# Kernel optimization log

Measured on AMD Instinct MI355X. Metric: run time of the kernel, lower is better.

The kernel has to match this reference:

```python
import jax, jax.numpy as jnp
import numpy as np

# BD-format field offsets (last dim = 512)
MARK_AX = 0
OPCODE_BASE = 16
OP_SHL = OPCODE_BASE + 23   # 39
OP_SHR = OPCODE_BASE + 24   # 40
ALU_LO = 64                 # 16-wide one-hot low nibble of operand
ALU_HI = 80                 # 16-wide one-hot high nibble of operand
AX_CARRY_LO = 96            # 16-wide one-hot shift amount
OUTPUT_LO = 128             # 16-wide result-low scatter target
OUTPUT_HI = 144             # 16-wide result-high scatter target

B, SEQ, D = 8, 32768, 512


def setup_inputs() -> dict:
    key = jax.random.key(0)
    ks = jax.random.split(key, 6)
    # background noise strictly below the 0.5 threshold so only intended bits fire
    x = jax.random.uniform(ks[0], (B, SEQ, D), dtype=jnp.float32) * 0.4
    mark = (jax.random.uniform(ks[1], (B, SEQ)) < 0.75).astype(jnp.float32)
    op_sel = jax.random.randint(ks[2], (B, SEQ), 0, 3)  # 0=none, 1=SHL, 2=SHR
    lo = jax.random.randint(ks[3], (B, SEQ), 0, 16)
    hi = jax.random.randint(ks[4], (B, SEQ), 0, 16)
    sa = jax.random.randint(ks[5], (B, SEQ), 0, 16)
    oh = lambda idx: jax.nn.one_hot(idx, 16, dtype=jnp.float32)
    x = x.at[..., MARK_AX].set(mark)
    x = x.at[..., OP_SHL].set((op_sel == 1).astype(jnp.float32))
    x = x.at[..., OP_SHR].set((op_sel == 2).astype(jnp.float32))
    x = x.at[..., ALU_LO:ALU_LO + 16].set(oh(lo))
    x = x.at[..., ALU_HI:ALU_HI + 16].set(oh(hi))
    x = x.at[..., AX_CARRY_LO:AX_CARRY_LO + 16].set(oh(sa))
    return {"x_bd": x}


def reference(x_bd):
    hot = x_bd > 0.5
    # 'first k with value > 0.5' == argmax over boolean (0 if none, matching torch default)
    first16 = lambda off: jnp.argmax(hot[..., off:off + 16], axis=-1).astype(jnp.int32)
    lo = first16(ALU_LO)          # [B,S] in [0,16)
    hi = first16(ALU_HI)
    sa = first16(AX_CARRY_LO)     # shift amount
    val = lo + 16 * hi            # 8-bit operand
    shl = jnp.left_shift(val, sa) & 0xFF   # SHL layer stack: 8-bit left shift
    shr = jnp.right_shift(val, sa)         # SHR layer stack: logical right shift
    mark = hot[..., MARK_AX]
    is_shl = hot[..., OP_SHL]
    is_shr = jnp.logical_and(hot[..., OP_SHR], jnp.logical_not(is_shl))  # elif priority
    act_shl = jnp.logical_and(mark, is_shl)
    act_shr = jnp.logical_and(mark, is_shr)
    active = jnp.logical_or(act_shl, act_shr)
    res = jnp.where(act_shl, shl, jnp.where(act_shr, shr, 0))
    res = jnp.clip(res, 0, 255)   # ge_to_bd clamps each nibble to [0,15]
    rlo = res & 15
    rhi = res >> 4
    amp = 2.0 * active.astype(x_bd.dtype)  # +2.0 scatter only for routed tokens
    add_lo = amp[..., None] * jax.nn.one_hot(rlo, 16, dtype=x_bd.dtype)
    add_hi = amp[..., None] * jax.nn.one_hot(rhi, 16, dtype=x_bd.dtype)
    out = x_bd.at[..., OUTPUT_LO:OUTPUT_LO + 16].add(add_lo)
    out = out.at[..., OUTPUT_HI:OUTPUT_HI + 16].add(add_hi)
    return out
```

## Files before the change

kernel.cpp:

```cpp
#include <hip/hip_runtime.h>

#define MARK_AX      0
#define OP_SHL       39
#define OP_SHR       40
#define ALU_LO       64
#define ALU_HI       80
#define AX_CARRY_LO  96
#define OUTPUT_LO    128
#define OUTPUT_HI    144

constexpr int D = 512;

__global__ __launch_bounds__(256) void shift_ffn_kernel(
    const float* __restrict__ x, float* __restrict__ out, int ntok)
{
    const int lane = threadIdx.x & 63;
    const int wid  = (blockIdx.x * blockDim.x + threadIdx.x) >> 6;
    const int nw   = (gridDim.x * blockDim.x) >> 6;
    const int e0   = 4 * lane;

    for (int tok = wid; tok < ntok; tok += nw) {
        const float* xt = x   + (size_t)tok * D;
        float*       ot = out + (size_t)tok * D;

        float4 a = *reinterpret_cast<const float4*>(xt + e0);
        float4 b = *reinterpret_cast<const float4*>(xt + 256 + e0);

        unsigned long long m = 0ull;
        if (lane < 28) {
            const float av[4] = {a.x, a.y, a.z, a.w};
            #pragma unroll
            for (int j = 0; j < 4; ++j) {
                const int e = e0 + j;
                if (av[j] > 0.5f) {
                    if (e == MARK_AX)                              m |= 1ull << 48;
                    else if (e == OP_SHL)                          m |= 1ull << 49;
                    else if (e == OP_SHR)                          m |= 1ull << 50;
                    else if (e >= ALU_LO      && e < ALU_LO + 16)  m |= 1ull << (e - ALU_LO);
                    else if (e >= ALU_HI      && e < ALU_HI + 16)  m |= 1ull << (e - ALU_HI + 16);
                    else if (e >= AX_CARRY_LO && e < AX_CARRY_LO+16) m |= 1ull << (e - AX_CARRY_LO + 32);
                }
            }
        }

        #pragma unroll
        for (int s = 1; s < 64; s <<= 1)
            m |= __shfl_xor(m, s, 64);

        const unsigned lo16 = (unsigned)( m        & 0xFFFFu);
        const unsigned hi16 = (unsigned)((m >> 16) & 0xFFFFu);
        const unsigned sa16 = (unsigned)((m >> 32) & 0xFFFFu);
        const int lo = lo16 ? (__ffs(lo16) - 1) : 0;
        const int hi = hi16 ? (__ffs(hi16) - 1) : 0;
        const int sa = sa16 ? (__ffs(sa16) - 1) : 0;

        const int  val     = lo + 16 * hi;
        const bool mark    = (m >> 48) & 1ull;
        const bool is_shl  = (m >> 49) & 1ull;
        const bool is_shr  = (((m >> 50) & 1ull) != 0) && !is_shl;
        const bool act_shl = mark && is_shl;
        const bool act_shr = mark && is_shr;
        const bool active  = act_shl || act_shr;

        int res = 0;
        if (act_shl)      res = (val << sa) & 0xFF;
        else if (act_shr) res = val >> sa;

        const int tlo = OUTPUT_LO + (res & 15);
        const int thi = OUTPUT_HI + (res >> 4);

        if (active) {
            float* ap = &a.x;
            #pragma unroll
            for (int j = 0; j < 4; ++j) {
                const int e = e0 + j;
                float add = 0.0f;
                if (e == tlo) add += 2.0f;
                if (e == thi) add += 2.0f;
                ap[j] += add;
            }
        }

        *reinterpret_cast<float4*>(ot + e0)       = a;
        *reinterpret_cast<float4*>(ot + 256 + e0) = b;
    }
}

extern "C" void kernel_launch(void* const* d_in, const int* in_sizes, int n_in,
                              void* d_out, int out_size, void* d_ws, size_t ws_size,
                              hipStream_t stream)
{
    const float* x = (const float*)d_in[0];
    float* out = (float*)d_out;
    const int ntok = in_sizes[0] / D;

    const int block = 256;
    const int grid  = 2048;
    shift_ffn_kernel<<<grid, block, 0, stream>>>(x, out, ntok);
}
```

Before: 209.9 us.

## Decode with wave ballots, process token pairs, use nontemporal loads/stores

```diff
diff --git a/kernel.cpp b/kernel.cpp
--- a/kernel.cpp
+++ b/kernel.cpp
@@ -11,6 +11,41 @@
 
 constexpr int D = 512;
 
+typedef float f32x4 __attribute__((ext_vector_type(4)));
+
+__device__ __forceinline__ int first_hot(const unsigned long long b[4], int lane0) {
+    int best = 999;
+    #pragma unroll
+    for (int j = 0; j < 4; ++j) {
+        unsigned nib = (unsigned)(b[j] >> lane0) & 0xFu;
+        int cand = nib ? (4 * (__ffs(nib) - 1) + j) : 999;
+        best = min(best, cand);
+    }
+    return (best >= 16) ? 0 : best;
+}
+
+__device__ __forceinline__ void decode(const unsigned long long b[4],
+                                       int& tlo, int& thi, float& amp) {
+    const bool mark = (b[0] >> 0) & 1ull;
+    const bool shl  = (b[3] >> 9) & 1ull;
+    const bool shr  = (b[0] >> 10) & 1ull;
+
+    const int lo = first_hot(b, 16);
+    const int hi = first_hot(b, 20);
+    const int sa = first_hot(b, 24);
+
+    const int  val     = lo + 16 * hi;
+    const bool act_shl = mark && shl;
+    const bool act_shr = mark && shr && !shl;
+
+    const int res = act_shl ? ((val << sa) & 0xFF)
+                  : (act_shr ? (val >> sa) : 0);
+
+    tlo = OUTPUT_LO + (res & 15);
+    thi = OUTPUT_HI + (res >> 4);
+    amp = (act_shl || act_shr) ? 2.0f : 0.0f;
+}
+
 __global__ __launch_bounds__(256) void shift_ffn_kernel(
     const float* __restrict__ x, float* __restrict__ out, int ntok)
 {
@@ -18,71 +53,38 @@
     const int wid  = (blockIdx.x * blockDim.x + threadIdx.x) >> 6;
     const int nw   = (gridDim.x * blockDim.x) >> 6;
     const int e0   = 4 * lane;
+    const int npair = ntok >> 1;
 
-    for (int tok = wid; tok < ntok; tok += nw) {
-        const float* xt = x   + (size_t)tok * D;
-        float*       ot = out + (size_t)tok * D;
+    for (int p = wid; p < npair; p += nw) {
+        const float* xt0 = x   + (size_t)(2 * p) * D;
+        float*       ot0 = out + (size_t)(2 * p) * D;
 
-        float4 a = *reinterpret_cast<const float4*>(xt + e0);
-        float4 b = *reinterpret_cast<const float4*>(xt + 256 + e0);
+        f32x4 a0 = __builtin_nontemporal_load((const f32x4*)(xt0 + e0));
+        f32x4 c0 = __builtin_nontemporal_load((const f32x4*)(xt0 + 256 + e0));
+        f32x4 a1 = __builtin_nontemporal_load((const f32x4*)(xt0 + D + e0));
+        f32x4 c1 = __builtin_nontemporal_load((const f32x4*)(xt0 + D + 256 + e0));
 
-        unsigned long long m = 0ull;
-        if (lane < 28) {
-            const float av[4] = {a.x, a.y, a.z, a.w};
-            #pragma unroll
-            for (int j = 0; j < 4; ++j) {
-                const int e = e0 + j;
-                if (av[j] > 0.5f) {
-                    if (e == MARK_AX)                              m |= 1ull << 48;
-                    else if (e == OP_SHL)                          m |= 1ull << 49;
-                    else if (e == OP_SHR)                          m |= 1ull << 50;
-                    else if (e >= ALU_LO      && e < ALU_LO + 16)  m |= 1ull << (e - ALU_LO);
-                    else if (e >= ALU_HI      && e < ALU_HI + 16)  m |= 1ull << (e - ALU_HI + 16);
-                    else if (e >= AX_CARRY_LO && e < AX_CARRY_LO+16) m |= 1ull << (e - AX_CARRY_LO + 32);
-                }
-            }
+        unsigned long long b0[4], b1[4];
+        #pragma unroll
+        for (int j = 0; j < 4; ++j) b0[j] = __ballot(a0[j] > 0.5f);
+        #pragma unroll
+        for (int j = 0; j < 4; ++j) b1[j] = __ballot(a1[j] > 0.5f);
+
+        int tlo0, thi0, tlo1, thi1; float amp0, amp1;
+        decode(b0, tlo0, thi0, amp0);
+        decode(b1, tlo1, thi1, amp1);
+
+        #pragma unroll
+        for (int j = 0; j < 4; ++j) {
+            const int e = e0 + j;
+            a0[j] += ((e == tlo0) ? amp0 : 0.0f) + ((e == thi0) ? amp0 : 0.0f);
+            a1[j] += ((e == tlo1) ? amp1 : 0.0f) + ((e == thi1) ? amp1 : 0.0f);
         }
 
-        #pragma unroll
-        for (int s = 1; s < 64; s <<= 1)
-            m |= __shfl_xor(m, s, 64);
-
-        const unsigned lo16 = (unsigned)( m        & 0xFFFFu);
-        const unsigned hi16 = (unsigned)((m >> 16) & 0xFFFFu);
-        const unsigned sa16 = (unsigned)((m >> 32) & 0xFFFFu);
-        const int lo = lo16 ? (__ffs(lo16) - 1) : 0;
-        const int hi = hi16 ? (__ffs(hi16) - 1) : 0;
-        const int sa = sa16 ? (__ffs(sa16) - 1) : 0;
-
-        const int  val     = lo + 16 * hi;
-        const bool mark    = (m >> 48) & 1ull;
-        const bool is_shl  = (m >> 49) & 1ull;
-        const bool is_shr  = (((m >> 50) & 1ull) != 0) && !is_shl;
-        const bool act_shl = mark && is_shl;
-        const bool act_shr = mark && is_shr;
-        const bool active  = act_shl || act_shr;
-
-        int res = 0;
-        if (act_shl)      res = (val << sa) & 0xFF;
-        else if (act_shr) res = val >> sa;
-
-        const int tlo = OUTPUT_LO + (res & 15);
-        const int thi = OUTPUT_HI + (res >> 4);
-
-        if (active) {
-            float* ap = &a.x;
-            #pragma unroll
-            for (int j = 0; j < 4; ++j) {
-                const int e = e0 + j;
-                float add = 0.0f;
-                if (e == tlo) add += 2.0f;
-                if (e == thi) add += 2.0f;
-                ap[j] += add;
-            }
-        }
-
-        *reinterpret_cast<float4*>(ot + e0)       = a;
-        *reinterpret_cast<float4*>(ot + 256 + e0) = b;
+        __builtin_nontemporal_store(a0, (f32x4*)(ot0 + e0));
+        __builtin_nontemporal_store(c0, (f32x4*)(ot0 + 256 + e0));
+        __builtin_nontemporal_store(a1, (f32x4*)(ot0 + D + e0));
+        __builtin_nontemporal_store(c1, (f32x4*)(ot0 + D + 256 + e0));
     }
 }
 
```

Result: faster. 188.2 us (-10.3%).
